# Kernel tuning notes

Hardware: AMD Instinct MI355X
Metric: run time of the kernel (lower is better)

Reference implementation:

```python
import math
import jax, jax.numpy as jnp
import numpy as np

EMBED_DIM = 1024
NUM_HEADS = 16
HEAD_DIM = EMBED_DIM // NUM_HEADS


def setup_inputs() -> dict:
    key = jax.random.key(0)
    kx, kqkv, kproj = jax.random.split(key, 3)
    b, sq, h = 2, 2048, EMBED_DIM
    x = jax.random.normal(kx, (b, sq, h), dtype=jnp.float32)
    # torch Linear weights are [out_features, in_features]
    # xavier_uniform for qkv: bound = sqrt(6/(fan_in+fan_out))
    bound_qkv = math.sqrt(6.0 / (h + 3 * h))
    Wqkv = jax.random.uniform(kqkv, (3 * h, h), dtype=jnp.float32,
                              minval=-bound_qkv, maxval=bound_qkv)
    # kaiming_uniform(a=sqrt(5)) for proj: bound = 1/sqrt(fan_in)
    bound_p = 1.0 / math.sqrt(h)
    Wproj = jax.random.uniform(kproj, (h, h), dtype=jnp.float32,
                               minval=-bound_p, maxval=bound_p)
    bproj = jnp.zeros((h,), dtype=jnp.float32)
    # self-attention: query == key == value (module asserts equality)
    return {"query": x, "key": x, "value": x,
            "Wqkv": Wqkv, "Wproj": Wproj, "bproj": bproj}


def reference(query, key, value, Wqkv, Wproj, bproj):
    b, sq, h = query.shape
    nh, hn = NUM_HEADS, HEAD_DIM
    # permute to [sq, b, h] then flatten tokens (seq-major)
    x = jnp.transpose(query, (1, 0, 2)).reshape(sq * b, h)
    qkv = x @ Wqkv.T                       # [sq*b, 3h] (no qkv bias: add_bias_kv=False)
    qkv = qkv.reshape(sq, b, nh, 3 * hn)
    q, k, v = jnp.split(qkv, 3, axis=-1)   # each [sq, b, nh, hn]
    # view to (sq, b*nh, hn) then transpose(0,1) -> [b*nh, sq, hn] (b-major, nh-minor)
    q = q.reshape(sq, b * nh, hn).transpose(1, 0, 2)
    k = k.reshape(sq, b * nh, hn).transpose(1, 0, 2)
    v = v.reshape(sq, b * nh, hn).transpose(1, 0, 2)
    scale = 1.0 / math.sqrt(hn)
    scores = jnp.einsum('nqd,nkd->nqk', q, k) * scale   # [b*nh, sq, sq] full matrix
    attn = jax.nn.softmax(scores, axis=-1)
    ctx = jnp.einsum('nqk,nkd->nqd', attn, v)           # [b*nh, sq, hn]
    # NOTE: original code views the b*nh (b-major) dim as (nh, b) -- reproduce exactly
    ctx = ctx.reshape(nh, b, sq, hn)
    ctx = jnp.transpose(ctx, (2, 1, 0, 3)).reshape(sq * b, h)
    out = ctx @ Wproj.T + bproj
    out = out.reshape(sq, b, h)
    return jnp.transpose(out, (1, 0, 2))   # [b, sq, h]
```

## Files before the change

### kernel.cpp

```cpp
#include <hip/hip_runtime.h>
#include <stdint.h>

#define B_   2
#define SQ   2048
#define H    1024
#define NH   16
#define HN   64
#define T_TOK 4096
#define N3H  3072

typedef __bf16 bf16x8 __attribute__((ext_vector_type(8)));
typedef float  f32x4  __attribute__((ext_vector_type(4)));

#define MFMA16(a, b, c) __builtin_amdgcn_mfma_f32_16x16x32_bf16((a), (b), (c), 0, 0, 0)

#define LGKM_DRAIN() do { \
  __builtin_amdgcn_s_waitcnt(0xC07F); \
  __builtin_amdgcn_wave_barrier(); \
} while (0)

__device__ __forceinline__ uint16_t f2bf_u(float f) {
  union { float f; uint32_t u; } v; v.f = f;
  uint32_t u = v.u;
  u += 0x7fffu + ((u >> 16) & 1u);
  return (uint16_t)(u >> 16);
}

__device__ __forceinline__ bf16x8 ldb8(const uint16_t* p) {
  return *reinterpret_cast<const bf16x8*>(p);
}

__device__ __forceinline__ void gll16(const uint16_t* g, uint16_t* l) {
  __builtin_amdgcn_global_load_lds(
      (const __attribute__((address_space(1))) uint32_t*)g,
      (__attribute__((address_space(3))) uint32_t*)l, 16, 0, 0);
}

__global__ __launch_bounds__(256) void convert_kernel(
    const float* __restrict__ x, const float* __restrict__ wqkv,
    const float* __restrict__ wproj,
    uint16_t* __restrict__ xb, uint16_t* __restrict__ wqkvb,
    uint16_t* __restrict__ wprojb) {
  const int XT4 = (T_TOK * H) / 4;
  const int WQ4 = (N3H * H) / 4;
  int i4 = blockIdx.x * 256 + threadIdx.x;
  const float* src;
  uint16_t* dst;
  if (i4 < XT4) {
    int i = i4 * 4;
    int t = i >> 10, c = i & 1023;
    int bi = t & 1, s = t >> 1;
    src = x + (bi * SQ + s) * H + c;
    dst = xb + i;
  } else if (i4 < XT4 + WQ4) {
    int j = (i4 - XT4) * 4;
    src = wqkv + j; dst = wqkvb + j;
  } else {
    int j = (i4 - XT4 - WQ4) * 4;
    src = wproj + j; dst = wprojb + j;
  }
  float4 v = *(const float4*)src;
  ushort4 o;
  o.x = f2bf_u(v.x); o.y = f2bf_u(v.y); o.z = f2bf_u(v.z); o.w = f2bf_u(v.w);
  *(ushort4*)dst = o;
}

__global__ __launch_bounds__(256) void gemm_qkv_kernel(
    const uint16_t* __restrict__ xb, const uint16_t* __restrict__ wb,
    uint16_t* __restrict__ Qb, uint16_t* __restrict__ Kb,
    uint16_t* __restrict__ Vtb) {
  const int lane = threadIdx.x & 63;
  const int wave = threadIdx.x >> 6;
  const int quad = lane >> 4, l16 = lane & 15;
  const int wm = wave >> 1, wn = wave & 1;
  const int row0 = blockIdx.y * 128, col0 = blockIdx.x * 128;

  __shared__ __align__(16) char smem[4 * 64 * 76 * 2];
  uint16_t* sA = (uint16_t*)smem;
  uint16_t* sB = (uint16_t*)(smem + 8192);
  uint16_t* W  = (uint16_t*)(smem) + wave * (64 * 76);

  const int lrow = lane >> 2;
  const int lk   = (lane & 3) * 8;

  f32x4 acc[4][4];
#pragma unroll
  for (int i = 0; i < 4; ++i)
#pragma unroll
    for (int j = 0; j < 4; ++j) acc[i][j] = (f32x4){0.f, 0.f, 0.f, 0.f};

  for (int k0 = 0; k0 < H; k0 += 32) {
#pragma unroll
    for (int c = 0; c < 2; ++c) {
      int g = c * 4 + wave;
      gll16(xb + (size_t)(row0 + g * 16 + lrow) * H + k0 + lk, sA + g * 512);
      gll16(wb + (size_t)(col0 + g * 16 + lrow) * H + k0 + lk, sB + g * 512);
    }
    __syncthreads();
    bf16x8 af[4], bfr[4];
#pragma unroll
    for (int mt = 0; mt < 4; ++mt)
      af[mt] = ldb8(sA + (wm * 64 + mt * 16 + l16) * 32 + quad * 8);
#pragma unroll
    for (int nt = 0; nt < 4; ++nt)
      bfr[nt] = ldb8(sB + (wn * 64 + nt * 16 + l16) * 32 + quad * 8);
#pragma unroll
    for (int mt = 0; mt < 4; ++mt)
#pragma unroll
      for (int nt = 0; nt < 4; ++nt)
        acc[mt][nt] = MFMA16(af[mt], bfr[nt], acc[mt][nt]);
    __syncthreads();
  }

  const int c0 = col0 + wn * 64;
  const int cm = c0 >> 6;
  const int hd = cm / 3;
  const int which = cm - hd * 3;
  const int t0 = row0 + wm * 64;

  if (which < 2) {
#pragma unroll
    for (int mt = 0; mt < 4; ++mt)
#pragma unroll
      for (int nt = 0; nt < 4; ++nt)
#pragma unroll
        for (int r = 0; r < 4; ++r)
          W[(mt * 16 + quad * 4 + r) * 76 + nt * 16 + l16] = f2bf_u(acc[mt][nt][r]);
    LGKM_DRAIN();
    uint16_t* dstb = (which == 0) ? Qb : Kb;
    const int t8 = lane >> 3, d0 = (lane & 7) * 8;
#pragma unroll
    for (int it = 0; it < 8; ++it) {
      int tl = it * 8 + t8;
      int t = t0 + tl;
      int s = t >> 1;
      int n = (t & 1) * NH + hd;
      bf16x8 vv = ldb8(W + tl * 76 + d0);
      *(bf16x8*)(dstb + (size_t)(n * SQ + s) * HN + d0) = vv;
    }
  } else {
    uint32_t* W32 = (uint32_t*)W;
#pragma unroll
    for (int mt = 0; mt < 4; ++mt)
#pragma unroll
      for (int nt = 0; nt < 4; ++nt) {
        int base = (nt * 16 + l16) * 76 + mt * 8 + quad * 2;
        W32[base >> 1] =
            (uint32_t)f2bf_u(acc[mt][nt][0]) | ((uint32_t)f2bf_u(acc[mt][nt][2]) << 16);
        W32[(base >> 1) + 16] =
            (uint32_t)f2bf_u(acc[mt][nt][1]) | ((uint32_t)f2bf_u(acc[mt][nt][3]) << 16);
      }
    LGKM_DRAIN();
    const int dl = lane >> 3;
    const int bi = (lane >> 2) & 1;
    const int sc = (lane & 3) * 8;
    const int s0 = (row0 >> 1) + wm * 32;
    const int n = bi * NH + hd;
#pragma unroll
    for (int it = 0; it < 8; ++it) {
      int d = it * 8 + dl;
      bf16x8 vv = ldb8(W + d * 76 + bi * 32 + sc);
      *(bf16x8*)(Vtb + (size_t)(n * HN + d) * SQ + s0 + sc) = vv;
    }
  }
}

__global__ __launch_bounds__(512, 6) void attn_kernel(
    const uint16_t* __restrict__ Qb, const uint16_t* __restrict__ Kb,
    const uint16_t* __restrict__ Vtb, uint16_t* __restrict__ ctxb) {
  const int lane = threadIdx.x & 63;
  const int wave = threadIdx.x >> 6;
  const int quad = lane >> 4, l16 = lane & 15;
  const int head  = blockIdx.x;
  const int qtile = blockIdx.y;
  const int wq = wave & 3;
  const int hf = wave >> 2;
  const int q0 = qtile * 64 + wq * 16;

  const uint16_t* Qh = Qb + (size_t)head * SQ * HN;
  const uint16_t* Kh = Kb + (size_t)head * SQ * HN;
  const uint16_t* Vh = Vtb + (size_t)head * HN * SQ;

  __shared__ __align__(16) char smem_raw[32768];
  uint16_t (*stage)[2][64][64] = (uint16_t(*)[2][64][64])smem_raw;
  float (*cacc)[64][21]        = (float(*)[64][21])smem_raw;
  uint16_t* pz = &stage[hf][0][wq * 16][0];

  const int lr8 = lane >> 3;
  const int lc8 = lane & 7;
  const int sc8 = (lc8 - lr8) & 7;

  bf16x8 aq0 = ldb8(Qh + (q0 + l16) * HN + quad * 8);
  bf16x8 aq1 = ldb8(Qh + (q0 + l16) * HN + 32 + quad * 8);

  float lrun[4];
  f32x4 acc[4];
#pragma unroll
  for (int r = 0; r < 4; ++r) {
    lrun[r] = 0.f;
    acc[r] = (f32x4){0.f, 0.f, 0.f, 0.f};
  }
  const float sc2 = 0.125f * 1.44269504f;

  for (int kt = 0; kt < 16; ++kt) {
    const int kbase = (hf * 16 + kt) * 64;
#pragma unroll
    for (int j = 0; j < 2; ++j) {
      int rr = wq * 16 + j * 8;
      gll16(Kh + (size_t)(kbase + rr + lr8) * HN + sc8 * 8, &stage[hf][0][rr][0]);
      gll16(Vh + (size_t)(rr + lr8) * SQ + kbase + sc8 * 8, &stage[hf][1][rr][0]);
    }
    __syncthreads();

    f32x4 s4[4];
#pragma unroll
    for (int st = 0; st < 4; ++st) {
      bf16x8 k0 = ldb8(&stage[hf][0][st * 16 + l16][0] + ((quad + l16) & 7) * 8);
      bf16x8 k1 = ldb8(&stage[hf][0][st * 16 + l16][0] + ((quad + 4 + l16) & 7) * 8);
      f32x4 z = (f32x4){0.f, 0.f, 0.f, 0.f};
      z = MFMA16(aq0, k0, z);
      s4[st] = MFMA16(aq1, k1, z);
    }
    __syncthreads();

#pragma unroll
    for (int st = 0; st < 4; ++st)
#pragma unroll
      for (int r = 0; r < 4; ++r) {
        float p = __builtin_amdgcn_exp2f(s4[st][r] * sc2);
        int row = quad * 4 + r;
        int phys = (st * 2 + (l16 >> 3) + row) & 7;
        pz[row * 64 + phys * 8 + (l16 & 7)] = f2bf_u(p);
        lrun[r] += p;
      }
    LGKM_DRAIN();
    bf16x8 ap0 = ldb8(pz + l16 * 64 + ((quad + l16) & 7) * 8);
    bf16x8 ap1 = ldb8(pz + l16 * 64 + ((quad + 4 + l16) & 7) * 8);
#pragma unroll
    for (int dt = 0; dt < 4; ++dt) {
      bf16x8 v0 = ldb8(&stage[hf][1][dt * 16 + l16][0] + ((quad + l16) & 7) * 8);
      bf16x8 v1 = ldb8(&stage[hf][1][dt * 16 + l16][0] + ((quad + 4 + l16) & 7) * 8);
      acc[dt] = MFMA16(ap0, v0, acc[dt]);
      acc[dt] = MFMA16(ap1, v1, acc[dt]);
    }
    __syncthreads();
  }

  if (hf) {
    float* dst = cacc[wq][lane];
#pragma unroll
    for (int dt = 0; dt < 4; ++dt)
#pragma unroll
      for (int r = 0; r < 4; ++r) dst[dt * 4 + r] = acc[dt][r];
#pragma unroll
    for (int r = 0; r < 4; ++r) dst[16 + r] = lrun[r];
  }
  __syncthreads();
  if (hf) return;
  {
    const float* src = cacc[wq][lane];
#pragma unroll
    for (int dt = 0; dt < 4; ++dt)
#pragma unroll
      for (int r = 0; r < 4; ++r) acc[dt][r] += src[dt * 4 + r];
#pragma unroll
    for (int r = 0; r < 4; ++r) lrun[r] += src[16 + r];
  }

  float rinv[4];
#pragma unroll
  for (int r = 0; r < 4; ++r) {
    float ls = lrun[r];
    ls += __shfl_xor(ls, 1);
    ls += __shfl_xor(ls, 2);
    ls += __shfl_xor(ls, 4);
    ls += __shfl_xor(ls, 8);
    rinv[r] = __builtin_amdgcn_rcpf(ls);
  }
#pragma unroll
  for (int dt = 0; dt < 4; ++dt)
#pragma unroll
    for (int r = 0; r < 4; ++r) {
      int qg = q0 + quad * 4 + r;
      int dg = dt * 16 + l16;
      float v = acc[dt][r] * rinv[r];
      int row = qg * 2 + (head & 1);
      int col = (head >> 1) * HN + dg;
      ctxb[row * H + col] = f2bf_u(v);
    }
}

__global__ __launch_bounds__(256) void gemm_proj_kernel(
    const uint16_t* __restrict__ ab, const uint16_t* __restrict__ wb,
    const float* __restrict__ bias, float* __restrict__ out) {
  const int lane = threadIdx.x & 63;
  const int wave = threadIdx.x >> 6;
  const int quad = lane >> 4, l16 = lane & 15;
  const int row0 = blockIdx.y * 128, col0 = blockIdx.x * 64;

  __shared__ __align__(16) uint16_t sA[128 * 32];
  __shared__ __align__(16) uint16_t sB[64 * 32];

  const int lrow = lane >> 2;
  const int lk   = (lane & 3) * 8;

  f32x4 acc[2][4];
#pragma unroll
  for (int i = 0; i < 2; ++i)
#pragma unroll
    for (int j = 0; j < 4; ++j) acc[i][j] = (f32x4){0.f, 0.f, 0.f, 0.f};

  for (int k0 = 0; k0 < H; k0 += 32) {
#pragma unroll
    for (int c = 0; c < 2; ++c) {
      int g = c * 4 + wave;
      gll16(ab + (size_t)(row0 + g * 16 + lrow) * H + k0 + lk, sA + g * 512);
    }
    gll16(wb + (size_t)(col0 + wave * 16 + lrow) * H + k0 + lk, sB + wave * 512);
    __syncthreads();
    bf16x8 af[2], bfr[4];
#pragma unroll
    for (int mt = 0; mt < 2; ++mt)
      af[mt] = ldb8(sA + (wave * 32 + mt * 16 + l16) * 32 + quad * 8);
#pragma unroll
    for (int nt = 0; nt < 4; ++nt)
      bfr[nt] = ldb8(sB + (nt * 16 + l16) * 32 + quad * 8);
#pragma unroll
    for (int mt = 0; mt < 2; ++mt)
#pragma unroll
      for (int nt = 0; nt < 4; ++nt)
        acc[mt][nt] = MFMA16(af[mt], bfr[nt], acc[mt][nt]);
    __syncthreads();
  }

#pragma unroll
  for (int mt = 0; mt < 2; ++mt)
#pragma unroll
    for (int nt = 0; nt < 4; ++nt)
#pragma unroll
      for (int r = 0; r < 4; ++r) {
        int m = row0 + wave * 32 + mt * 16 + quad * 4 + r;
        int c = col0 + nt * 16 + l16;
        int s = m >> 1, bi = m & 1;
        out[(size_t)(bi * SQ + s) * H + c] = acc[mt][nt][r] + bias[c];
      }
}

extern "C" void kernel_launch(void* const* d_in, const int* in_sizes, int n_in,
                              void* d_out, int out_size, void* d_ws, size_t ws_size,
                              hipStream_t stream) {
  const float* x     = (const float*)d_in[0];
  const float* wqkv  = (const float*)d_in[3];
  const float* wproj = (const float*)d_in[4];
  const float* bproj = (const float*)d_in[5];
  float* out = (float*)d_out;

  char* ws = (char*)d_ws;
  uint16_t* xb     = (uint16_t*)(ws);
  uint16_t* wqkvb  = (uint16_t*)(ws + (8ull  << 20));
  uint16_t* wprojb = (uint16_t*)(ws + (14ull << 20));
  uint16_t* Qb     = (uint16_t*)(ws + (16ull << 20));
  uint16_t* Kb     = (uint16_t*)(ws + (24ull << 20));
  uint16_t* Vtb    = (uint16_t*)(ws + (32ull << 20));
  uint16_t* ctxb   = (uint16_t*)(ws + (40ull << 20));

  convert_kernel<<<8192, 256, 0, stream>>>(x, wqkv, wproj, xb, wqkvb, wprojb);
  gemm_qkv_kernel<<<dim3(N3H / 128, T_TOK / 128), 256, 0, stream>>>(xb, wqkvb, Qb, Kb, Vtb);
  attn_kernel<<<dim3(B_ * NH, SQ / 64), 512, 0, stream>>>(Qb, Kb, Vtb, ctxb);
  gemm_proj_kernel<<<dim3(H / 64, T_TOK / 128), 256, 0, stream>>>(ctxb, wprojb, bproj, out);
}
```

Baseline: 232.2 us.

## Give each attention wave two 16-row query groups to reuse K/V fragments

The attention block drops from 8 waves to 4. Each wave now handles 32 query rows as two 16-row groups, so every K and V fragment read from shared memory feeds two MFMAs instead of one. This halves LDS traffic for K/V per unit of work and puts fewer waves on each barrier. In exchange, register pressure roughly doubles for accumulators and scores, occupancy per block drops, and each wave issues more global loads per tile.

```diff
diff --git a/kernel.cpp b/kernel.cpp
--- a/kernel.cpp
+++ b/kernel.cpp
@@ -165,7 +165,7 @@
   }
 }
 
-__global__ __launch_bounds__(512, 6) void attn_kernel(
+__global__ __launch_bounds__(256, 4) void attn_kernel(
     const uint16_t* __restrict__ Qb, const uint16_t* __restrict__ Kb,
     const uint16_t* __restrict__ Vtb, uint16_t* __restrict__ ctxb) {
   const int lane = threadIdx.x & 63;
@@ -173,121 +173,152 @@
   const int quad = lane >> 4, l16 = lane & 15;
   const int head  = blockIdx.x;
   const int qtile = blockIdx.y;
-  const int wq = wave & 3;
-  const int hf = wave >> 2;
-  const int q0 = qtile * 64 + wq * 16;
+  const int wq = wave & 1;
+  const int hf = wave >> 1;
+  const int q0 = qtile * 64 + wq * 32;
 
   const uint16_t* Qh = Qb + (size_t)head * SQ * HN;
   const uint16_t* Kh = Kb + (size_t)head * SQ * HN;
   const uint16_t* Vh = Vtb + (size_t)head * HN * SQ;
 
   __shared__ __align__(16) char smem_raw[32768];
-  uint16_t (*stage)[2][64][64] = (uint16_t(*)[2][64][64])smem_raw;
-  float (*cacc)[64][21]        = (float(*)[64][21])smem_raw;
-  uint16_t* pz = &stage[hf][0][wq * 16][0];
+  uint16_t (*stageK)[64][64] = (uint16_t(*)[64][64])smem_raw;
+  uint16_t (*stageV)[64][64] = (uint16_t(*)[64][64])(smem_raw + 16384);
+  float (*cacc)[64][41]      = (float(*)[64][41])smem_raw;
+  uint16_t* pz = &stageK[hf][wq * 32][0];
 
   const int lr8 = lane >> 3;
   const int lc8 = lane & 7;
   const int sc8 = (lc8 - lr8) & 7;
 
-  bf16x8 aq0 = ldb8(Qh + (q0 + l16) * HN + quad * 8);
-  bf16x8 aq1 = ldb8(Qh + (q0 + l16) * HN + 32 + quad * 8);
-
-  float lrun[4];
-  f32x4 acc[4];
-#pragma unroll
-  for (int r = 0; r < 4; ++r) {
-    lrun[r] = 0.f;
-    acc[r] = (f32x4){0.f, 0.f, 0.f, 0.f};
-  }
+  bf16x8 aq[2][2];
+#pragma unroll
+  for (int g = 0; g < 2; ++g)
+#pragma unroll
+    for (int h = 0; h < 2; ++h)
+      aq[g][h] = ldb8(Qh + (q0 + g * 16 + l16) * HN + h * 32 + quad * 8);
+
+  float lrun[2][4];
+  f32x4 acc[2][4];
+#pragma unroll
+  for (int g = 0; g < 2; ++g)
+#pragma unroll
+    for (int r = 0; r < 4; ++r) {
+      lrun[g][r] = 0.f;
+      acc[g][r] = (f32x4){0.f, 0.f, 0.f, 0.f};
+    }
   const float sc2 = 0.125f * 1.44269504f;
 
   for (int kt = 0; kt < 16; ++kt) {
     const int kbase = (hf * 16 + kt) * 64;
 #pragma unroll
-    for (int j = 0; j < 2; ++j) {
-      int rr = wq * 16 + j * 8;
-      gll16(Kh + (size_t)(kbase + rr + lr8) * HN + sc8 * 8, &stage[hf][0][rr][0]);
-      gll16(Vh + (size_t)(rr + lr8) * SQ + kbase + sc8 * 8, &stage[hf][1][rr][0]);
-    }
-    __syncthreads();
-
-    f32x4 s4[4];
+    for (int j = 0; j < 4; ++j) {
+      int rr = wq * 32 + j * 8;
+      gll16(Kh + (size_t)(kbase + rr + lr8) * HN + sc8 * 8, &stageK[hf][rr][0]);
+      gll16(Vh + (size_t)(rr + lr8) * SQ + kbase + sc8 * 8, &stageV[hf][rr][0]);
+    }
+    __syncthreads();
+
+    f32x4 s4[2][4];
 #pragma unroll
     for (int st = 0; st < 4; ++st) {
-      bf16x8 k0 = ldb8(&stage[hf][0][st * 16 + l16][0] + ((quad + l16) & 7) * 8);
-      bf16x8 k1 = ldb8(&stage[hf][0][st * 16 + l16][0] + ((quad + 4 + l16) & 7) * 8);
-      f32x4 z = (f32x4){0.f, 0.f, 0.f, 0.f};
-      z = MFMA16(aq0, k0, z);
-      s4[st] = MFMA16(aq1, k1, z);
-    }
-    __syncthreads();
-
-#pragma unroll
-    for (int st = 0; st < 4; ++st)
-#pragma unroll
-      for (int r = 0; r < 4; ++r) {
-        float p = __builtin_amdgcn_exp2f(s4[st][r] * sc2);
-        int row = quad * 4 + r;
-        int phys = (st * 2 + (l16 >> 3) + row) & 7;
-        pz[row * 64 + phys * 8 + (l16 & 7)] = f2bf_u(p);
-        lrun[r] += p;
+      bf16x8 k0 = ldb8(&stageK[hf][st * 16 + l16][0] + ((quad + l16) & 7) * 8);
+      bf16x8 k1 = ldb8(&stageK[hf][st * 16 + l16][0] + ((quad + 4 + l16) & 7) * 8);
+#pragma unroll
+      for (int g = 0; g < 2; ++g) {
+        f32x4 z = (f32x4){0.f, 0.f, 0.f, 0.f};
+        z = MFMA16(aq[g][0], k0, z);
+        s4[g][st] = MFMA16(aq[g][1], k1, z);
       }
+    }
+    __syncthreads();
+
+#pragma unroll
+    for (int g = 0; g < 2; ++g)
+#pragma unroll
+      for (int st = 0; st < 4; ++st)
+#pragma unroll
+        for (int r = 0; r < 4; ++r) {
+          float p = __builtin_amdgcn_exp2f(s4[g][st][r] * sc2);
+          int row = g * 16 + quad * 4 + r;
+          int phys = (st * 2 + (l16 >> 3) + row) & 7;
+          pz[row * 64 + phys * 8 + (l16 & 7)] = f2bf_u(p);
+          lrun[g][r] += p;
+        }
     LGKM_DRAIN();
-    bf16x8 ap0 = ldb8(pz + l16 * 64 + ((quad + l16) & 7) * 8);
-    bf16x8 ap1 = ldb8(pz + l16 * 64 + ((quad + 4 + l16) & 7) * 8);
+    bf16x8 ap[2][2];
+#pragma unroll
+    for (int g = 0; g < 2; ++g)
+#pragma unroll
+      for (int h = 0; h < 2; ++h)
+        ap[g][h] = ldb8(pz + (g * 16 + l16) * 64 + ((h * 4 + quad + l16) & 7) * 8);
 #pragma unroll
     for (int dt = 0; dt < 4; ++dt) {
-      bf16x8 v0 = ldb8(&stage[hf][1][dt * 16 + l16][0] + ((quad + l16) & 7) * 8);
-      bf16x8 v1 = ldb8(&stage[hf][1][dt * 16 + l16][0] + ((quad + 4 + l16) & 7) * 8);
-      acc[dt] = MFMA16(ap0, v0, acc[dt]);
-      acc[dt] = MFMA16(ap1, v1, acc[dt]);
+      bf16x8 v0 = ldb8(&stageV[hf][dt * 16 + l16][0] + ((quad + l16) & 7) * 8);
+      bf16x8 v1 = ldb8(&stageV[hf][dt * 16 + l16][0] + ((quad + 4 + l16) & 7) * 8);
+#pragma unroll
+      for (int g = 0; g < 2; ++g) {
+        acc[g][dt] = MFMA16(ap[g][0], v0, acc[g][dt]);
+        acc[g][dt] = MFMA16(ap[g][1], v1, acc[g][dt]);
+      }
     }
     __syncthreads();
   }
 
   if (hf) {
-    float* dst = cacc[wq][lane];
-#pragma unroll
-    for (int dt = 0; dt < 4; ++dt)
-#pragma unroll
-      for (int r = 0; r < 4; ++r) dst[dt * 4 + r] = acc[dt][r];
-#pragma unroll
-    for (int r = 0; r < 4; ++r) dst[16 + r] = lrun[r];
+    float* dst = &cacc[wq][lane][0];
+#pragma unroll
+    for (int g = 0; g < 2; ++g)
+#pragma unroll
+      for (int dt = 0; dt < 4; ++dt)
+#pragma unroll
+        for (int r = 0; r < 4; ++r) dst[g * 16 + dt * 4 + r] = acc[g][dt][r];
+#pragma unroll
+    for (int g = 0; g < 2; ++g)
+#pragma unroll
+      for (int r = 0; r < 4; ++r) dst[32 + g * 4 + r] = lrun[g][r];
   }
   __syncthreads();
   if (hf) return;
   {
-    const float* src = cacc[wq][lane];
+    const float* src = &cacc[wq][lane][0];
+#pragma unroll
+    for (int g = 0; g < 2; ++g)
+#pragma unroll
+      for (int dt = 0; dt < 4; ++dt)
+#pragma unroll
+        for (int r = 0; r < 4; ++r) acc[g][dt][r] += src[g * 16 + dt * 4 + r];
+#pragma unroll
+    for (int g = 0; g < 2; ++g)
+#pragma unroll
+      for (int r = 0; r < 4; ++r) lrun[g][r] += src[32 + g * 4 + r];
+  }
+
+  float rinv[2][4];
+#pragma unroll
+  for (int g = 0; g < 2; ++g)
+#pragma unroll
+    for (int r = 0; r < 4; ++r) {
+      float ls = lrun[g][r];
+      ls += __shfl_xor(ls, 1);
+      ls += __shfl_xor(ls, 2);
+      ls += __shfl_xor(ls, 4);
+      ls += __shfl_xor(ls, 8);
+      rinv[g][r] = __builtin_amdgcn_rcpf(ls);
+    }
+#pragma unroll
+  for (int g = 0; g < 2; ++g)
 #pragma unroll
     for (int dt = 0; dt < 4; ++dt)
 #pragma unroll
-      for (int r = 0; r < 4; ++r) acc[dt][r] += src[dt * 4 + r];
-#pragma unroll
-    for (int r = 0; r < 4; ++r) lrun[r] += src[16 + r];
-  }
-
-  float rinv[4];
-#pragma unroll
-  for (int r = 0; r < 4; ++r) {
-    float ls = lrun[r];
-    ls += __shfl_xor(ls, 1);
-    ls += __shfl_xor(ls, 2);
-    ls += __shfl_xor(ls, 4);
-    ls += __shfl_xor(ls, 8);
-    rinv[r] = __builtin_amdgcn_rcpf(ls);
-  }
-#pragma unroll
-  for (int dt = 0; dt < 4; ++dt)
-#pragma unroll
-    for (int r = 0; r < 4; ++r) {
-      int qg = q0 + quad * 4 + r;
-      int dg = dt * 16 + l16;
-      float v = acc[dt][r] * rinv[r];
-      int row = qg * 2 + (head & 1);
-      int col = (head >> 1) * HN + dg;
-      ctxb[row * H + col] = f2bf_u(v);
-    }
+      for (int r = 0; r < 4; ++r) {
+        int qg = q0 + g * 16 + quad * 4 + r;
+        int dg = dt * 16 + l16;
+        float v = acc[g][dt][r] * rinv[g][r];
+        int row = qg * 2 + (head & 1);
+        int col = (head >> 1) * HN + dg;
+        ctxb[row * H + col] = f2bf_u(v);
+      }
 }
 
 __global__ __launch_bounds__(256) void gemm_proj_kernel(
@@ -366,6 +397,6 @@
 
   convert_kernel<<<8192, 256, 0, stream>>>(x, wqkv, wproj, xb, wqkvb, wprojb);
   gemm_qkv_kernel<<<dim3(N3H / 128, T_TOK / 128), 256, 0, stream>>>(xb, wqkvb, Qb, Kb, Vtb);
-  attn_kernel<<<dim3(B_ * NH, SQ / 64), 512, 0, stream>>>(Qb, Kb, Vtb, ctxb);
+  attn_kernel<<<dim3(B_ * NH, SQ / 64), 256, 0, stream>>>(Qb, Kb, Vtb, ctxb);
   gemm_proj_kernel<<<dim3(H / 64, T_TOK / 128), 256, 0, stream>>>(ctxb, wprojb, bproj, out);
 }
```

Result: slower. 245.9 us (+5.9%).
